# Kernel optimization log

Measured on AMD Instinct MI355X. Metric: run time of the kernel, lower is better.

The kernel has to match this reference:

```python
import jax, jax.numpy as jnp
import numpy as np

# ---- static config (mirrors init_kwargs) ----
WIN_X, WIN_Y = 12, 12
GRID_X, GRID_Y = 468, 468
BATCH = 4
SHIFTS = ((0, 0), (6, 6))
MAX_WIN_X = GRID_X // WIN_X + 1            # 40
MAX_WIN_Y = GRID_Y // WIN_Y + 1            # 40
MAX_WIN_PER_SAMPLE = MAX_WIN_X * MAX_WIN_Y # 1600
# (level, max_tokens, drop_range_lo, drop_range_hi)
DROP_INFO = ((0, 30, 0, 30), (1, 60, 30, 60), (2, 100, 60, 100000))
SENTINEL = 2_000_000_000  # window id for masked-out voxels (sorts to the end)


def _window_partition(coors):
    # coors: [N,4] = [b, z, y, x] int32 -> batch-unique window index per shift
    out = []
    for sx, sy in SHIFTS:
        x = coors[:, 3] + sx
        y = coors[:, 2] + sy
        wx = x // WIN_X
        wy = y // WIN_Y
        out.append((coors[:, 0] * MAX_WIN_PER_SAMPLE + wx * MAX_WIN_Y + wy).astype(jnp.int32))
    return out


def _sort_group_stats(win):
    # inner index within each equal-value group (counting-sort style) and group size per element
    order = jnp.argsort(win)                      # stable
    s = win[order]
    n = win.shape[0]
    left_s = jnp.searchsorted(s, s, side='left')
    inner_sorted = jnp.arange(n, dtype=win.dtype) - left_s.astype(win.dtype)
    inner = jnp.zeros_like(win).at[order].set(inner_sorted)
    counts = (jnp.searchsorted(s, win, side='right') - jnp.searchsorted(s, win, side='left')).astype(win.dtype)
    return inner, counts


def _drop_single_shift(win, valid):
    # equivalent of SSTInputLayer.drop_single_shift restricted to `valid` voxels
    w = jnp.where(valid, win, SENTINEL)
    inner, counts = _sort_group_stats(w)
    target = jnp.zeros_like(w)
    lvl = -jnp.ones_like(w)
    for dl, max_tok, lo, hi in DROP_INFO:
        m = (counts >= lo) & (counts < hi)
        target = jnp.where(m, max_tok, target)
        lvl = jnp.where(m, dl, lvl)
    keep = valid & (inner < target)
    return keep, jnp.where(valid, lvl, -1)


def _make_continuous(w):
    # dense-rank of window ids (make_continuous_inds) over a sentinel-masked array
    order = jnp.argsort(w)
    s = w[order]
    new_grp = jnp.concatenate([jnp.zeros((1,), w.dtype), (s[1:] != s[:-1]).astype(w.dtype)])
    rank = jnp.cumsum(new_grp)
    return jnp.zeros_like(w).at[order].set(rank)


def _flat2win(win, keep, lvl):
    # per-voxel position in the [num_windows, max_tokens] buffer of its drop level; -1 if dropped
    out = -jnp.ones_like(win)
    for dl, max_tok, _, _ in DROP_INFO:
        valid = keep & (lvl == dl)
        w = jnp.where(valid, win, SENTINEL)
        conti = _make_continuous(w)
        inner, _ = _sort_group_stats(w)
        out = jnp.where(valid, conti * max_tok + inner, out)
    return out


def reference(voxel_feat, coors):
    coors = coors.astype(jnp.int32)
    bwi0, bwi1 = _window_partition(coors)
    n = voxel_feat.shape[0]
    all_valid = jnp.ones((n,), bool)
    keep0, lvl0 = _drop_single_shift(bwi0, all_valid)
    keep1, lvl1 = _drop_single_shift(bwi1, keep0)   # shift-1 drop computed among shift-0 survivors
    keep = keep0 & keep1
    feat = jnp.where(keep[:, None], voxel_feat, 0.0)  # fixed-shape analogue of voxel_feat[voxel_keep_inds]
    f2w0 = _flat2win(bwi0, keep, lvl0)
    f2w1 = _flat2win(bwi1, keep, lvl1)
    return feat, keep, lvl0, lvl1, bwi0, bwi1, f2w0, f2w1


def setup_inputs() -> dict:
    key = jax.random.key(0)
    k1, k2, k3, k4 = jax.random.split(key, 4)
    n, c = 300000, 128
    voxel_feat = jax.random.normal(k1, (n, c), dtype=jnp.float32)
    b = jax.random.randint(k2, (n,), 0, BATCH)
    y = jax.random.randint(k3, (n,), 0, GRID_Y)
    x = jax.random.randint(k4, (n,), 0, GRID_X)
    z = jnp.zeros((n,), jnp.int32)
    coors = jnp.stack([b, z, y, x], axis=1).astype(jnp.int32)
    return {"voxel_feat": voxel_feat, "coors": coors}
```

## Files before the change

kernel.cpp:

```cpp
#include <hip/hip_runtime.h>


#define NWIN 6400
#define CAP 128

__device__ __forceinline__ int targ_of(int k) {
    return (k < 30) ? 30 : (k < 60) ? 60 : (k < 100000) ? 100 : 0;
}
__device__ __forceinline__ int lvl_of(int k) {
    return (k < 30) ? 0 : (k < 60) ? 1 : (k < 100000) ? 2 : -1;
}

__global__ void k_zero(int* __restrict__ z) {
    int i = blockIdx.x * 256 + threadIdx.x;
    if (i < 3 * NWIN) z[i] = 0;
}

__global__ void __launch_bounds__(256) k_winscat(
    const int4* __restrict__ c4, int n,
    int* __restrict__ w0a, int* __restrict__ w1a,
    int* __restrict__ cnt0, int* __restrict__ seg0) {
    int i = blockIdx.x * 256 + threadIdx.x;
    if (i >= n) return;
    int4 c = c4[i];
    int w0 = c.x * 1600 + (c.w / 12) * 40 + (c.z / 12);
    int w1 = c.x * 1600 + ((c.w + 6) / 12) * 40 + ((c.z + 6) / 12);
    w0a[i] = w0;
    w1a[i] = w1;
    int p = atomicAdd(&cnt0[w0], 1);
    if (p < CAP) seg0[w0 * CAP + p] = i;
}

__global__ void __launch_bounds__(256) k_rank0(
    const int* __restrict__ cnt0, const int* __restrict__ seg0,
    const int* __restrict__ w0a, const int* __restrict__ w1a, int n,
    int* __restrict__ keep0, int* __restrict__ cnt1, int* __restrict__ seg1) {
    int w = blockIdx.x * 4 + (threadIdx.x >> 6);
    int lane = threadIdx.x & 63;
    int k = cnt0[w];
    if (k == 0) return;
    int target = targ_of(k);
    const int* s = seg0 + w * CAP;
    if (k <= 64) {
        int v = (lane < k) ? s[lane] : 0x7FFFFFFF;
        int r = 0;
        for (int j = 0; j < k; j++) { int b = __shfl(v, j, 64); r += (b < v) ? 1 : 0; }
        if (lane < k) {
            int kp = (r < target) ? 1 : 0;
            keep0[v] = kp;
            if (kp) {
                int w1 = w1a[v];
                int p = atomicAdd(&cnt1[w1], 1);
                if (p < CAP) seg1[w1 * CAP + p] = v;
            }
        }
    } else if (k <= CAP) {
        int k2 = k - 64;
        int v0 = s[lane];
        int v1 = (lane < k2) ? s[64 + lane] : 0x7FFFFFFF;
        int r0 = 0, r1 = 0;
        for (int j = 0; j < 64; j++) { int b = __shfl(v0, j, 64); r0 += (b < v0); r1 += (b < v1); }
        for (int j = 0; j < k2; j++) { int b = __shfl(v1, j, 64); r0 += (b < v0); r1 += (b < v1); }
        {
            int kp = (r0 < target) ? 1 : 0;
            keep0[v0] = kp;
            if (kp) { int w1 = w1a[v0]; int p = atomicAdd(&cnt1[w1], 1); if (p < CAP) seg1[w1 * CAP + p] = v0; }
        }
        if (lane < k2) {
            int kp = (r1 < target) ? 1 : 0;
            keep0[v1] = kp;
            if (kp) { int w1 = w1a[v1]; int p = atomicAdd(&cnt1[w1], 1); if (p < CAP) seg1[w1 * CAP + p] = v1; }
        }
    } else {
        if (lane == 0) {
            int c = 0;
            for (int i = 0; i < n; i++) {
                if (w0a[i] == w) {
                    int kp = (c < target) ? 1 : 0;
                    keep0[i] = kp;
                    if (kp) { int w1 = w1a[i]; int p = atomicAdd(&cnt1[w1], 1); if (p < CAP) seg1[w1 * CAP + p] = i; }
                    c++;
                }
            }
        }
    }
}

__global__ void __launch_bounds__(256) k_rank1(
    const int* __restrict__ cnt1, const int* __restrict__ seg1,
    const int* __restrict__ w0a, const int* __restrict__ w1a,
    const int* __restrict__ keep0, int n,
    int* __restrict__ keepF, int* __restrict__ rk1,
    int* __restrict__ keptC1, int* __restrict__ keptC0) {
    int w = blockIdx.x * 4 + (threadIdx.x >> 6);
    int lane = threadIdx.x & 63;
    int k = cnt1[w];
    int target = targ_of(k);
    if (lane == 0) keptC1[w] = (k < target) ? k : target;
    if (k == 0) return;
    const int* s = seg1 + w * CAP;
    if (k <= 64) {
        int v = (lane < k) ? s[lane] : 0x7FFFFFFF;
        int r = 0;
        for (int j = 0; j < k; j++) { int b = __shfl(v, j, 64); r += (b < v) ? 1 : 0; }
        if (lane < k) {
            int kp = (r < target) ? 1 : 0;
            keepF[v] = kp;
            if (kp) { rk1[v] = r; atomicAdd(&keptC0[w0a[v]], 1); }
        }
    } else if (k <= CAP) {
        int k2 = k - 64;
        int v0 = s[lane];
        int v1 = (lane < k2) ? s[64 + lane] : 0x7FFFFFFF;
        int r0 = 0, r1 = 0;
        for (int j = 0; j < 64; j++) { int b = __shfl(v0, j, 64); r0 += (b < v0); r1 += (b < v1); }
        for (int j = 0; j < k2; j++) { int b = __shfl(v1, j, 64); r0 += (b < v0); r1 += (b < v1); }
        {
            int kp = (r0 < target) ? 1 : 0;
            keepF[v0] = kp;
            if (kp) { rk1[v0] = r0; atomicAdd(&keptC0[w0a[v0]], 1); }
        }
        if (lane < k2) {
            int kp = (r1 < target) ? 1 : 0;
            keepF[v1] = kp;
            if (kp) { rk1[v1] = r1; atomicAdd(&keptC0[w0a[v1]], 1); }
        }
    } else {
        if (lane == 0) {
            int c = 0;
            for (int i = 0; i < n; i++) {
                if (w1a[i] == w && keep0[i]) {
                    int kp = (c < target) ? 1 : 0;
                    keepF[i] = kp;
                    if (kp) { rk1[i] = c; atomicAdd(&keptC0[w0a[i]], 1); }
                    c++;
                }
            }
        }
    }
}

__global__ void __launch_bounds__(256) k_rank0kept(
    const int* __restrict__ cnt0, const int* __restrict__ seg0,
    const int* __restrict__ keep0, const int* __restrict__ keepF,
    const int* __restrict__ w0a, int n, int* __restrict__ rk0) {
    int w = blockIdx.x * 4 + (threadIdx.x >> 6);
    int lane = threadIdx.x & 63;
    int k = cnt0[w];
    if (k == 0) return;
    const int* s = seg0 + w * CAP;
    if (k <= 64) {
        int v = 0x3FFFFFFF, f = 0;
        if (lane < k) { v = s[lane]; f = (keep0[v] && keepF[v]) ? 1 : 0; }
        int enc = v | (f << 30);
        int r = 0;
        for (int j = 0; j < k; j++) {
            int b = __shfl(enc, j, 64);
            r += ((b >> 30) & 1) & (int)((b & 0x3FFFFFFF) < v);
        }
        if (f) rk0[v] = r;
    } else if (k <= CAP) {
        int k2 = k - 64;
        int v0 = s[lane];
        int f0 = (keep0[v0] && keepF[v0]) ? 1 : 0;
        int v1 = 0x3FFFFFFF, f1 = 0;
        if (lane < k2) { v1 = s[64 + lane]; f1 = (keep0[v1] && keepF[v1]) ? 1 : 0; }
        int e0 = v0 | (f0 << 30), e1 = v1 | (f1 << 30);
        int r0 = 0, r1 = 0;
        for (int j = 0; j < 64; j++) {
            int b = __shfl(e0, j, 64);
            int bf = (b >> 30) & 1, bv = b & 0x3FFFFFFF;
            r0 += bf & (int)(bv < v0);
            r1 += bf & (int)(bv < v1);
        }
        for (int j = 0; j < k2; j++) {
            int b = __shfl(e1, j, 64);
            int bf = (b >> 30) & 1, bv = b & 0x3FFFFFFF;
            r0 += bf & (int)(bv < v0);
            r1 += bf & (int)(bv < v1);
        }
        if (f0) rk0[v0] = r0;
        if (f1) rk0[v1] = r1;
    } else {
        if (lane == 0) {
            int c = 0;
            for (int i = 0; i < n; i++) {
                if (w0a[i] == w && keep0[i] && keepF[i]) { rk0[i] = c; c++; }
            }
        }
    }
}

__global__ void k_conti2(
    const int* __restrict__ cnt0, const int* __restrict__ keptC0, int* __restrict__ conti0,
    const int* __restrict__ cnt1, const int* __restrict__ keptC1, int* __restrict__ conti1) {
    __shared__ int pc0[256], pc1[256], pc2[256];
    const int* cnt   = blockIdx.x ? cnt1 : cnt0;
    const int* keptC = blockIdx.x ? keptC1 : keptC0;
    int* conti       = blockIdx.x ? conti1 : conti0;
    int t = threadIdx.x;
    int st = t * 25;
    int c0 = 0, c1 = 0, c2 = 0;
    for (int j = 0; j < 25; j++) {
        int w = st + j;
        if (keptC[w] > 0) {
            int l = lvl_of(cnt[w]);
            c0 += (l == 0); c1 += (l == 1); c2 += (l == 2);
        }
    }
    pc0[t] = c0; pc1[t] = c1; pc2[t] = c2;
    __syncthreads();
    if (t == 0) {
        int a = 0, b = 0, c = 0;
        for (int j = 0; j < 256; j++) {
            int v0 = pc0[j], v1 = pc1[j], v2 = pc2[j];
            pc0[j] = a; pc1[j] = b; pc2[j] = c;
            a += v0; b += v1; c += v2;
        }
    }
    __syncthreads();
    int a0 = pc0[t], a1 = pc1[t], a2 = pc2[t];
    for (int j = 0; j < 25; j++) {
        int w = st + j;
        int l = lvl_of(cnt[w]);
        conti[w] = (l == 0) ? a0 : (l == 1) ? a1 : (l == 2) ? a2 : 0;
        if (keptC[w] > 0) {
            if (l == 0) a0++; else if (l == 1) a1++; else if (l == 2) a2++;
        }
    }
}

__global__ void __launch_bounds__(256) k_finalfeat(
    int n, const int* __restrict__ w0a, const int* __restrict__ w1a,
    const int* __restrict__ keep0, const int* __restrict__ keepF,
    const int* __restrict__ cnt0, const int* __restrict__ cnt1,
    const int* __restrict__ conti0, const int* __restrict__ conti1,
    const int* __restrict__ rk0, const int* __restrict__ rk1,
    const float4* __restrict__ feat, float* __restrict__ out, int nbScalar) {
    if ((int)blockIdx.x < nbScalar) {
        int i = blockIdx.x * 256 + threadIdx.x;
        if (i >= n) return;
        size_t N = (size_t)n;
        float* o = out + N * 128;
        int w0 = w0a[i], w1 = w1a[i];
        int k0 = keep0[i];
        int kf = (k0 && keepF[i]) ? 1 : 0;
        int l0 = lvl_of(cnt0[w0]);
        int l1 = k0 ? lvl_of(cnt1[w1]) : -1;
        int f0 = -1, f1 = -1;
        if (kf) {
            int mt0 = (l0 == 0) ? 30 : (l0 == 1) ? 60 : 100;
            int mt1 = (l1 == 0) ? 30 : (l1 == 1) ? 60 : 100;
            f0 = conti0[w0] * mt0 + rk0[i];
            f1 = conti1[w1] * mt1 + rk1[i];
        }
        o[i]         = (float)kf;
        o[N + i]     = (float)l0;
        o[2 * N + i] = (float)l1;
        o[3 * N + i] = (float)w0;
        o[4 * N + i] = (float)w1;
        o[5 * N + i] = (float)f0;
        o[6 * N + i] = (float)f1;
    } else {
        int gid = (blockIdx.x - nbScalar) * 256 + threadIdx.x;
        int total = n * 32;
        if (gid >= total) return;
        int row = gid >> 5;
        float4 v = feat[gid];
        if (!(keep0[row] && keepF[row])) { v.x = 0.f; v.y = 0.f; v.z = 0.f; v.w = 0.f; }
        ((float4*)out)[gid] = v;
    }
}

extern "C" void kernel_launch(void* const* d_in, const int* in_sizes, int n_in,
                              void* d_out, int out_size, void* d_ws, size_t ws_size,
                              hipStream_t stream) {
    (void)n_in; (void)out_size; (void)ws_size;
    const float* feat = (const float*)d_in[0];
    const int* coors  = (const int*)d_in[1];
    int n = in_sizes[1] / 4;
    float* out = (float*)d_out;
    int* ws = (int*)d_ws;

    int* cnt0   = ws;
    int* cnt1   = ws + 6400;
    int* keptC0 = ws + 12800;
    int* keptC1 = ws + 19200;
    int* conti0 = ws + 25600;
    int* conti1 = ws + 32000;
    int* w0a    = ws + 38400;
    int* w1a    = w0a + n;
    int* keep0  = w1a + n;
    int* keepF  = keep0 + n;
    int* rk0    = keepF + n;
    int* rk1    = rk0 + n;
    int* seg0   = rk1 + n;
    int* seg1   = seg0 + NWIN * CAP;

    int nb = (n + 255) / 256;
    int fb = (n * 32 + 255) / 256;

    k_zero<<<(3 * NWIN + 255) / 256, 256, 0, stream>>>(cnt0);
    k_winscat<<<nb, 256, 0, stream>>>((const int4*)coors, n, w0a, w1a, cnt0, seg0);
    k_rank0<<<NWIN / 4, 256, 0, stream>>>(cnt0, seg0, w0a, w1a, n, keep0, cnt1, seg1);
    k_rank1<<<NWIN / 4, 256, 0, stream>>>(cnt1, seg1, w0a, w1a, keep0, n,
                                          keepF, rk1, keptC1, keptC0);
    k_rank0kept<<<NWIN / 4, 256, 0, stream>>>(cnt0, seg0, keep0, keepF, w0a, n, rk0);
    k_conti2<<<2, 256, 0, stream>>>(cnt0, keptC0, conti0, cnt1, keptC1, conti1);
    k_finalfeat<<<nb + fb, 256, 0, stream>>>(n, w0a, w1a, keep0, keepF, cnt0, cnt1,
                                             conti0, conti1, rk0, rk1,
                                             (const float4*)feat, out, nb);
}
```

Measured before the change: 396.1 us.

## Compute shift-0 rank early and fix up only for shift-1 drops

Instead of a separate k_rank0kept pass that re-ranks every shift-0 window among final survivors, k_rank0 now records the provisional rank, and k_rank1 appends voxels dropped at shift 1 to a global drop list. A new k_fix kernel runs the two conti scans in its first two blocks and uses the remaining blocks to decrement the ranks of later survivors in each dropped voxel's window with atomics. This saves one kernel launch and a full pass over all windows, at the cost of a global atomic counter and atomic fix-ups whose amount grows with the number of drops.

New measurement: 390.2 us. Within noise of the previous version (-1.5%).

```diff
diff --git a/kernel.cpp b/kernel.cpp
--- a/kernel.cpp
+++ b/kernel.cpp
@@ -13,7 +13,7 @@
 
 __global__ void k_zero(int* __restrict__ z) {
     int i = blockIdx.x * 256 + threadIdx.x;
-    if (i < 3 * NWIN) z[i] = 0;
+    if (i < 3 * NWIN + 1) z[i] = 0;
 }
 
 __global__ void __launch_bounds__(256) k_winscat(
@@ -34,7 +34,8 @@
 __global__ void __launch_bounds__(256) k_rank0(
     const int* __restrict__ cnt0, const int* __restrict__ seg0,
     const int* __restrict__ w0a, const int* __restrict__ w1a, int n,
-    int* __restrict__ keep0, int* __restrict__ cnt1, int* __restrict__ seg1) {
+    int* __restrict__ keep0, int* __restrict__ rk0,
+    int* __restrict__ cnt1, int* __restrict__ seg1) {
     int w = blockIdx.x * 4 + (threadIdx.x >> 6);
     int lane = threadIdx.x & 63;
     int k = cnt0[w];
@@ -49,6 +50,7 @@
             int kp = (r < target) ? 1 : 0;
             keep0[v] = kp;
             if (kp) {
+                rk0[v] = r;
                 int w1 = w1a[v];
                 int p = atomicAdd(&cnt1[w1], 1);
                 if (p < CAP) seg1[w1 * CAP + p] = v;
@@ -64,12 +66,20 @@
         {
             int kp = (r0 < target) ? 1 : 0;
             keep0[v0] = kp;
-            if (kp) { int w1 = w1a[v0]; int p = atomicAdd(&cnt1[w1], 1); if (p < CAP) seg1[w1 * CAP + p] = v0; }
+            if (kp) {
+                rk0[v0] = r0;
+                int w1 = w1a[v0]; int p = atomicAdd(&cnt1[w1], 1);
+                if (p < CAP) seg1[w1 * CAP + p] = v0;
+            }
         }
         if (lane < k2) {
             int kp = (r1 < target) ? 1 : 0;
             keep0[v1] = kp;
-            if (kp) { int w1 = w1a[v1]; int p = atomicAdd(&cnt1[w1], 1); if (p < CAP) seg1[w1 * CAP + p] = v1; }
+            if (kp) {
+                rk0[v1] = r1;
+                int w1 = w1a[v1]; int p = atomicAdd(&cnt1[w1], 1);
+                if (p < CAP) seg1[w1 * CAP + p] = v1;
+            }
         }
     } else {
         if (lane == 0) {
@@ -78,7 +88,11 @@
                 if (w0a[i] == w) {
                     int kp = (c < target) ? 1 : 0;
                     keep0[i] = kp;
-                    if (kp) { int w1 = w1a[i]; int p = atomicAdd(&cnt1[w1], 1); if (p < CAP) seg1[w1 * CAP + p] = i; }
+                    if (kp) {
+                        rk0[i] = c;
+                        int w1 = w1a[i]; int p = atomicAdd(&cnt1[w1], 1);
+                        if (p < CAP) seg1[w1 * CAP + p] = i;
+                    }
                     c++;
                 }
             }
@@ -91,7 +105,8 @@
     const int* __restrict__ w0a, const int* __restrict__ w1a,
     const int* __restrict__ keep0, int n,
     int* __restrict__ keepF, int* __restrict__ rk1,
-    int* __restrict__ keptC1, int* __restrict__ keptC0) {
+    int* __restrict__ keptC1, int* __restrict__ keptC0,
+    int* __restrict__ dropCnt, int* __restrict__ droplist) {
     int w = blockIdx.x * 4 + (threadIdx.x >> 6);
     int lane = threadIdx.x & 63;
     int k = cnt1[w];
@@ -107,6 +122,7 @@
             int kp = (r < target) ? 1 : 0;
             keepF[v] = kp;
             if (kp) { rk1[v] = r; atomicAdd(&keptC0[w0a[v]], 1); }
+            else    { int d = atomicAdd(dropCnt, 1); droplist[d] = v; }
         }
     } else if (k <= CAP) {
         int k2 = k - 64;
@@ -119,11 +135,13 @@
             int kp = (r0 < target) ? 1 : 0;
             keepF[v0] = kp;
             if (kp) { rk1[v0] = r0; atomicAdd(&keptC0[w0a[v0]], 1); }
+            else    { int d = atomicAdd(dropCnt, 1); droplist[d] = v0; }
         }
         if (lane < k2) {
             int kp = (r1 < target) ? 1 : 0;
             keepF[v1] = kp;
             if (kp) { rk1[v1] = r1; atomicAdd(&keptC0[w0a[v1]], 1); }
+            else    { int d = atomicAdd(dropCnt, 1); droplist[d] = v1; }
         }
     } else {
         if (lane == 0) {
@@ -133,6 +151,7 @@
                     int kp = (c < target) ? 1 : 0;
                     keepF[i] = kp;
                     if (kp) { rk1[i] = c; atomicAdd(&keptC0[w0a[i]], 1); }
+                    else    { int d = atomicAdd(dropCnt, 1); droplist[d] = i; }
                     c++;
                 }
             }
@@ -140,64 +159,9 @@
     }
 }
 
-__global__ void __launch_bounds__(256) k_rank0kept(
-    const int* __restrict__ cnt0, const int* __restrict__ seg0,
-    const int* __restrict__ keep0, const int* __restrict__ keepF,
-    const int* __restrict__ w0a, int n, int* __restrict__ rk0) {
-    int w = blockIdx.x * 4 + (threadIdx.x >> 6);
-    int lane = threadIdx.x & 63;
-    int k = cnt0[w];
-    if (k == 0) return;
-    const int* s = seg0 + w * CAP;
-    if (k <= 64) {
-        int v = 0x3FFFFFFF, f = 0;
-        if (lane < k) { v = s[lane]; f = (keep0[v] && keepF[v]) ? 1 : 0; }
-        int enc = v | (f << 30);
-        int r = 0;
-        for (int j = 0; j < k; j++) {
-            int b = __shfl(enc, j, 64);
-            r += ((b >> 30) & 1) & (int)((b & 0x3FFFFFFF) < v);
-        }
-        if (f) rk0[v] = r;
-    } else if (k <= CAP) {
-        int k2 = k - 64;
-        int v0 = s[lane];
-        int f0 = (keep0[v0] && keepF[v0]) ? 1 : 0;
-        int v1 = 0x3FFFFFFF, f1 = 0;
-        if (lane < k2) { v1 = s[64 + lane]; f1 = (keep0[v1] && keepF[v1]) ? 1 : 0; }
-        int e0 = v0 | (f0 << 30), e1 = v1 | (f1 << 30);
-        int r0 = 0, r1 = 0;
-        for (int j = 0; j < 64; j++) {
-            int b = __shfl(e0, j, 64);
-            int bf = (b >> 30) & 1, bv = b & 0x3FFFFFFF;
-            r0 += bf & (int)(bv < v0);
-            r1 += bf & (int)(bv < v1);
-        }
-        for (int j = 0; j < k2; j++) {
-            int b = __shfl(e1, j, 64);
-            int bf = (b >> 30) & 1, bv = b & 0x3FFFFFFF;
-            r0 += bf & (int)(bv < v0);
-            r1 += bf & (int)(bv < v1);
-        }
-        if (f0) rk0[v0] = r0;
-        if (f1) rk0[v1] = r1;
-    } else {
-        if (lane == 0) {
-            int c = 0;
-            for (int i = 0; i < n; i++) {
-                if (w0a[i] == w && keep0[i] && keepF[i]) { rk0[i] = c; c++; }
-            }
-        }
-    }
-}
-
-__global__ void k_conti2(
-    const int* __restrict__ cnt0, const int* __restrict__ keptC0, int* __restrict__ conti0,
-    const int* __restrict__ cnt1, const int* __restrict__ keptC1, int* __restrict__ conti1) {
-    __shared__ int pc0[256], pc1[256], pc2[256];
-    const int* cnt   = blockIdx.x ? cnt1 : cnt0;
-    const int* keptC = blockIdx.x ? keptC1 : keptC0;
-    int* conti       = blockIdx.x ? conti1 : conti0;
+__device__ __forceinline__ void conti_scan(
+    const int* __restrict__ cnt, const int* __restrict__ keptC,
+    int* __restrict__ conti, int* pc0, int* pc1, int* pc2) {
     int t = threadIdx.x;
     int st = t * 25;
     int c0 = 0, c1 = 0, c2 = 0;
@@ -226,6 +190,39 @@
         conti[w] = (l == 0) ? a0 : (l == 1) ? a1 : (l == 2) ? a2 : 0;
         if (keptC[w] > 0) {
             if (l == 0) a0++; else if (l == 1) a1++; else if (l == 2) a2++;
+        }
+    }
+}
+
+__global__ void k_fix(
+    const int* __restrict__ cnt0, const int* __restrict__ keptC0, int* __restrict__ conti0,
+    const int* __restrict__ cnt1, const int* __restrict__ keptC1, int* __restrict__ conti1,
+    const int* __restrict__ dropCnt, const int* __restrict__ droplist,
+    const int* __restrict__ w0a, const int* __restrict__ seg0,
+    const int* __restrict__ keep0, const int* __restrict__ keepF,
+    int* __restrict__ rk0, int n) {
+    __shared__ int pc0[256], pc1[256], pc2[256];
+    if (blockIdx.x == 0) { conti_scan(cnt0, keptC0, conti0, pc0, pc1, pc2); return; }
+    if (blockIdx.x == 1) { conti_scan(cnt1, keptC1, conti1, pc0, pc1, pc2); return; }
+    int nd = *dropCnt;
+    if (nd == 0) return;
+    int waveId = (blockIdx.x - 2) * 4 + (threadIdx.x >> 6);
+    int nWaves = (gridDim.x - 2) * 4;
+    int lane = threadIdx.x & 63;
+    for (int e = waveId; e < nd; e += nWaves) {
+        int u = droplist[e];
+        int w = w0a[u];
+        int k = cnt0[w];
+        if (k <= CAP) {
+            const int* s = seg0 + w * CAP;
+            for (int j = lane; j < k; j += 64) {
+                int v = s[j];
+                if (v > u && keep0[v] && keepF[v]) atomicSub(&rk0[v], 1);
+            }
+        } else if (lane == 0) {
+            for (int i = u + 1; i < n; i++) {
+                if (w0a[i] == w && keep0[i] && keepF[i]) atomicSub(&rk0[i], 1);
+            }
         }
     }
 }
@@ -282,31 +279,36 @@
     float* out = (float*)d_out;
     int* ws = (int*)d_ws;
 
-    int* cnt0   = ws;
-    int* cnt1   = ws + 6400;
-    int* keptC0 = ws + 12800;
-    int* keptC1 = ws + 19200;
-    int* conti0 = ws + 25600;
-    int* conti1 = ws + 32000;
-    int* w0a    = ws + 38400;
-    int* w1a    = w0a + n;
-    int* keep0  = w1a + n;
-    int* keepF  = keep0 + n;
-    int* rk0    = keepF + n;
-    int* rk1    = rk0 + n;
-    int* seg0   = rk1 + n;
-    int* seg1   = seg0 + NWIN * CAP;
+    int* cnt0     = ws;
+    int* cnt1     = ws + 6400;
+    int* keptC0   = ws + 12800;
+    int* dropCnt  = ws + 19200;
+    int* keptC1   = ws + 25600;
+    int* conti0   = ws + 32000;
+    int* conti1   = ws + 38400;
+    int* droplist = ws + 44800;
+    int* w0a      = droplist + n;
+    int* w1a      = w0a + n;
+    int* keep0    = w1a + n;
+    int* keepF    = keep0 + n;
+    int* rk0      = keepF + n;
+    int* rk1      = rk0 + n;
+    int* seg0     = rk1 + n;
+    int* seg1     = seg0 + NWIN * CAP;
 
     int nb = (n + 255) / 256;
     int fb = (n * 32 + 255) / 256;
 
-    k_zero<<<(3 * NWIN + 255) / 256, 256, 0, stream>>>(cnt0);
+    k_zero<<<(3 * NWIN + 1 + 255) / 256, 256, 0, stream>>>(cnt0);
     k_winscat<<<nb, 256, 0, stream>>>((const int4*)coors, n, w0a, w1a, cnt0, seg0);
-    k_rank0<<<NWIN / 4, 256, 0, stream>>>(cnt0, seg0, w0a, w1a, n, keep0, cnt1, seg1);
+    k_rank0<<<NWIN / 4, 256, 0, stream>>>(cnt0, seg0, w0a, w1a, n,
+                                          keep0, rk0, cnt1, seg1);
     k_rank1<<<NWIN / 4, 256, 0, stream>>>(cnt1, seg1, w0a, w1a, keep0, n,
-                                          keepF, rk1, keptC1, keptC0);
-    k_rank0kept<<<NWIN / 4, 256, 0, stream>>>(cnt0, seg0, keep0, keepF, w0a, n, rk0);
-    k_conti2<<<2, 256, 0, stream>>>(cnt0, keptC0, conti0, cnt1, keptC1, conti1);
+                                          keepF, rk1, keptC1, keptC0,
+                                          dropCnt, droplist);
+    k_fix<<<66, 256, 0, stream>>>(cnt0, keptC0, conti0, cnt1, keptC1, conti1,
+                                  dropCnt, droplist, w0a, seg0, keep0, keepF,
+                                  rk0, n);
     k_finalfeat<<<nb + fb, 256, 0, stream>>>(n, w0a, w1a, keep0, keepF, cnt0, cnt1,
                                              conti0, conti1, rk0, rk1,
                                              (const float4*)feat, out, nb);
```
